# Kernel optimization log

Measured on AMD Instinct MI355X. Metric: run time of the kernel, lower is better.

## Reference

```python
import jax, jax.numpy as jnp
import numpy as np

N, E, DIN, H, DOUT = 100000, 400000, 128, 128, 128
LN_EPS = 1e-5


def _layernorm(x, g, b):
    m = jnp.mean(x, axis=-1, keepdims=True)
    v = jnp.mean((x - m) ** 2, axis=-1, keepdims=True)
    return (x - m) * jax.lax.rsqrt(v + LN_EPS) * g + b


def setup_inputs() -> dict:
    key = jax.random.key(0)
    ks = jax.random.split(key, 24)
    s = 1.0 / np.sqrt(H)
    inp = {
        'feat': jax.random.normal(ks[0], (N, DIN), jnp.float32),
        'edge_src': jax.random.randint(ks[1], (E,), 0, N, jnp.int32),
        'edge_dst': jax.random.randint(ks[2], (E,), 0, N, jnp.int32),
        'W_src': jax.random.normal(ks[3], (DIN, H), jnp.float32) * s,
        'b_src': jax.random.normal(ks[4], (H,), jnp.float32) * s,
        'W_dst': jax.random.normal(ks[5], (DIN, H), jnp.float32) * s,
        'b_dst': jax.random.normal(ks[6], (H,), jnp.float32) * s,
        'W1a': jax.random.normal(ks[7], (H, H), jnp.float32) * s,
        'W1b': jax.random.normal(ks[8], (H, H), jnp.float32) * s,
        'b1': jax.random.normal(ks[9], (H,), jnp.float32) * s,
        'W2': jax.random.normal(ks[10], (H, H), jnp.float32) * s,
        'b2': jax.random.normal(ks[11], (H,), jnp.float32) * s,
        'W3': jax.random.normal(ks[12], (H, H), jnp.float32) * s,
        'b3': jax.random.normal(ks[13], (H,), jnp.float32) * s,
        'ln_g': jnp.ones((H,), jnp.float32),
        'ln_b': jnp.zeros((H,), jnp.float32),
        'Wg1a': jax.random.normal(ks[14], (H, H), jnp.float32) * s,
        'Wg1b': jax.random.normal(ks[15], (H, H), jnp.float32) * s,
        'bg1': jax.random.normal(ks[16], (H,), jnp.float32) * s,
        'Wg2': jax.random.normal(ks[17], (H, 1), jnp.float32) * s,
        'bg2': jax.random.normal(ks[18], (1,), jnp.float32) * s,
        'W_out': jax.random.normal(ks[19], (H, DOUT), jnp.float32) * s,
        'b_out': jax.random.normal(ks[20], (DOUT,), jnp.float32) * s,
    }
    return inp


def reference(feat, edge_src, edge_dst, W_src, b_src, W_dst, b_dst,
              W1a, W1b, b1, W2, b2, W3, b3, ln_g, ln_b,
              Wg1a, Wg1b, bg1, Wg2, bg2, W_out, b_out):
    gelu = lambda x: jax.nn.gelu(x, approximate=False)  # torch nn.GELU default (erf)
    # node-level src/dst transforms, then gather per edge
    src_h = feat @ W_src + b_src                 # [N,H]
    dst_h = feat @ W_dst + b_dst                 # [N,H]
    se = src_h[edge_src]                         # [E,H]
    de = dst_h[edge_dst]                         # [E,H]
    # edge MLP on concat([se,de]) expressed as split weights (same math)
    h = gelu(se @ W1a + de @ W1b + b1)           # [E,H]
    h = gelu(h @ W2 + b2)                        # [E,H]
    msg = _layernorm(h @ W3 + b3, ln_g, ln_b)    # [E,H]
    # message gating
    gate = jax.nn.sigmoid(gelu(se @ Wg1a + de @ Wg1b + bg1) @ Wg2 + bg2)  # [E,1]
    msg = gate * msg
    # scatter-sum to destination nodes, then out transform
    upd = jax.ops.segment_sum(msg, edge_dst, num_segments=N)  # [N,H]
    return upd @ W_out + b_out                   # [N,DOUT]
```

## Files before the change

### kernel.cpp

```cpp
#include <hip/hip_runtime.h>
#include <hip/hip_bf16.h>
#include <math.h>


typedef __bf16 bf16x8 __attribute__((ext_vector_type(8)));
typedef __bf16 bf16x2 __attribute__((ext_vector_type(2)));
typedef float floatx4 __attribute__((ext_vector_type(4)));

#define LN_EPS 1e-5f

__device__ __forceinline__ unsigned short f2bf(float x) {
  unsigned int u = __float_as_uint(x);
  u = u + 0x7fffu + ((u >> 16) & 1u);
  return (unsigned short)(u >> 16);
}

__device__ __forceinline__ unsigned int pkbf(float lo, float hi) {
  bf16x2 v;
  v.x = (__bf16)lo;
  v.y = (__bf16)hi;
  return __builtin_bit_cast(unsigned int, v);
}

__device__ __forceinline__ unsigned short f2bfh(float x) {
  __bf16 h = (__bf16)x;
  return __builtin_bit_cast(unsigned short, h);
}

__device__ __forceinline__ float bf2f(unsigned short s) {
  return __uint_as_float(((unsigned int)s) << 16);
}

__device__ __forceinline__ float geluf(float x) {
  float t = x * x;
  float u = x * (2.3022080f + 0.1029434f * t);
  float e = __builtin_amdgcn_exp2f(-u);
  return x * __builtin_amdgcn_rcpf(1.0f + e);
}

__device__ __forceinline__ float sigmoidf_fast(float x) {
  float e = __builtin_amdgcn_exp2f(-1.44269504f * x);
  return __builtin_amdgcn_rcpf(1.0f + e);
}

__global__ __launch_bounds__(256) void prep_weights(
    const float* w0, const float* w1, const float* w2, const float* w3,
    const float* w4, const float* w5, const float* w6, const float* w7,
    const float* w8, unsigned short* out) {
  const float* srcs[9] = {w0, w1, w2, w3, w4, w5, w6, w7, w8};
  int m = blockIdx.x >> 2, c = blockIdx.x & 3;
  const float* src = srcs[m] + c * 32 * 128;
  __shared__ unsigned short sT[128][35];
  int tid = threadIdx.x;

  for (int it = 0; it < 4; ++it) {
    int f4 = tid + it * 256;
    float4 v = ((const float4*)src)[f4];
    int krel = f4 >> 5;
    int n0 = (f4 & 31) * 4;
    sT[n0 + 0][krel] = f2bf(v.x);
    sT[n0 + 1][krel] = f2bf(v.y);
    sT[n0 + 2][krel] = f2bf(v.z);
    sT[n0 + 3][krel] = f2bf(v.w);
  }
  __syncthreads();
  unsigned short* dst = out + m * 16384 + c * 32;
  for (int it = 0; it < 2; ++it) {
    int ch = tid + it * 256;
    int n = ch >> 2, kc = (ch & 3) * 8;
    unsigned short tmp[8];
    for (int j = 0; j < 8; ++j) tmp[j] = sT[n][kc + j];
    *(int4*)(dst + n * 128 + kc) = *(const int4*)tmp;
  }
}

#define LDB(pB, B)                                              \
  do {                                                          \
    const unsigned short* _p = (pB);                            \
    for (int kb = 0; kb < 4; ++kb) {                            \
      B[0][kb] = *(const bf16x8*)(_p + kb * 32);                \
      B[1][kb] = *(const bf16x8*)(_p + 2048 + kb * 32);         \
    }                                                           \
  } while (0)

__global__ __launch_bounds__(512, 8) void node_fused(
    const float* __restrict__ feat, const unsigned short* __restrict__ wT,
    const float* __restrict__ b_src, const float* __restrict__ b_dst,
    const float* __restrict__ b1, const float* __restrict__ bg1,
    unsigned short* __restrict__ SrcCat, unsigned short* __restrict__ DstCat,
    unsigned short* __restrict__ upd, int M) {
  __shared__ __align__(16) unsigned short sF[64][136];
  __shared__ __align__(16) unsigned short sT[64][136];
  int tid = threadIdx.x;
  int r0 = blockIdx.x * 64;
  int y = blockIdx.y;

  if (y == 0) {
    int4 z = {0, 0, 0, 0};
    int4* p = (int4*)(upd + (long long)r0 * 128);
    for (int it = 0; it < 2; ++it) {
      int idx = tid + it * 512;
      if (r0 + (idx >> 4) < M) p[idx] = z;
    }
  }

  {
    int r = tid >> 3, seg = tid & 7;
    int row = r0 + r;
    const float* src = feat + (long long)row * 128 + seg * 16;
    if (row < M) {
      float4 f0 = *(const float4*)(src);
      float4 f1 = *(const float4*)(src + 4);
      float4 f2 = *(const float4*)(src + 8);
      float4 f3 = *(const float4*)(src + 12);
      unsigned int t0[4] = {pkbf(f0.x, f0.y), pkbf(f0.z, f0.w),
                            pkbf(f1.x, f1.y), pkbf(f1.z, f1.w)};
      unsigned int t1[4] = {pkbf(f2.x, f2.y), pkbf(f2.z, f2.w),
                            pkbf(f3.x, f3.y), pkbf(f3.z, f3.w)};
      *(int4*)&sF[r][seg * 16] = *(const int4*)t0;
      *(int4*)&sF[r][seg * 16 + 8] = *(const int4*)t1;
    } else {
      int4 z = {0, 0, 0, 0};
      *(int4*)&sF[r][seg * 16] = z;
      *(int4*)&sF[r][seg * 16 + 8] = z;
    }
  }
  __syncthreads();

  int w = tid >> 6;
  int lane = tid & 63, lr = lane & 15, q = lane >> 4;
  int c0 = 16 * w + lr;
  const unsigned short* pB = wT + c0 * 128 + q * 8;

  const unsigned short* wH = pB + (y ? 1 : 0) * 16384;
  const unsigned short* wA = pB + (y ? 3 : 2) * 16384;
  const unsigned short* wG = pB + (y ? 7 : 6) * 16384;
  unsigned short* Cat = y ? DstCat : SrcCat;
  float hb = y ? b_dst[c0] : b_src[c0];
  float ab = y ? 0.f : b1[c0];
  float gb = y ? 0.f : bg1[c0];

  bf16x8 B[4];
  floatx4 acc[4];

  auto ldb = [&](const unsigned short* p) {
#pragma unroll
    for (int kb = 0; kb < 4; ++kb) B[kb] = *(const bf16x8*)(p + kb * 32);
  };
  auto zacc = [&]() {
#pragma unroll
    for (int mb = 0; mb < 4; ++mb) acc[mb] = (floatx4){0.f, 0.f, 0.f, 0.f};
  };
  auto pass = [&](const unsigned short (*Ab)[136]) {
#pragma unroll
    for (int kb = 0; kb < 4; ++kb) {
      int k = kb * 32 + q * 8;
#pragma unroll
      for (int mb = 0; mb < 4; ++mb) {
        bf16x8 a = *(const bf16x8*)&Ab[16 * mb + lr][k];
        acc[mb] = __builtin_amdgcn_mfma_f32_16x16x32_bf16(a, B[kb], acc[mb], 0, 0, 0);
      }
    }
  };
  auto stage = [&](unsigned short (*S)[136], float bv) {
#pragma unroll
    for (int mb = 0; mb < 4; ++mb)
#pragma unroll
      for (int i = 0; i < 4; ++i)
        S[16 * mb + 4 * q + i][c0] = f2bfh(acc[mb][i] + bv);
  };

  ldb(wH); zacc(); pass(sF); stage(sT, hb);
  __syncthreads();

  ldb(wA); zacc(); pass(sT); stage(sF, ab);
  ldb(wG); zacc(); pass(sT);
  __syncthreads();
  stage(sT, gb);
  __syncthreads();

  for (int it = 0; it < 4; ++it) {
    int idx = tid + it * 512;
    int row = idx >> 5, c = idx & 31;
    if (r0 + row < M) {
      const void* src = (c < 16) ? (const void*)&sF[row][c * 8]
                                 : (const void*)&sT[row][(c - 16) * 8];
      *(int4*)(Cat + (long long)(r0 + row) * 256 + c * 8) = *(const int4*)src;
    }
  }
}

__global__ __launch_bounds__(512, 8) void gemm_out(
    const unsigned short* __restrict__ A, const unsigned short* __restrict__ Bt,
    const float* __restrict__ bias, float* __restrict__ C, int M) {
  __shared__ __align__(16) char smem[64 * 130 * 4];
  unsigned short (*sA)[136] = (unsigned short(*)[136])smem;
  float (*sO)[130] = (float(*)[130])smem;
  int tid = threadIdx.x;
  int r0 = blockIdx.x * 64;

  for (int it = 0; it < 2; ++it) {
    int idx = tid + it * 512;
    int row = idx >> 4, c = idx & 15;
    int4 v = {0, 0, 0, 0};
    if (r0 + row < M) v = ((const int4*)(A + (long long)(r0 + row) * 128))[c];
    *(int4*)&sA[row][c * 8] = v;
  }
  __syncthreads();

  int w = tid >> 6, lane = tid & 63, lr = lane & 15, q = lane >> 4;
  int c0 = 16 * w + lr;
  const unsigned short* pB = Bt + c0 * 128 + q * 8;

  bf16x8 B[4];
#pragma unroll
  for (int kb = 0; kb < 4; ++kb) B[kb] = *(const bf16x8*)(pB + kb * 32);
  floatx4 acc[4];
#pragma unroll
  for (int mb = 0; mb < 4; ++mb) acc[mb] = (floatx4){0.f, 0.f, 0.f, 0.f};
#pragma unroll
  for (int kb = 0; kb < 4; ++kb) {
    int k = kb * 32 + q * 8;
#pragma unroll
    for (int mb = 0; mb < 4; ++mb) {
      bf16x8 a = *(const bf16x8*)&sA[16 * mb + lr][k];
      acc[mb] = __builtin_amdgcn_mfma_f32_16x16x32_bf16(a, B[kb], acc[mb], 0, 0, 0);
    }
  }
  __syncthreads();

  float bv = bias[c0];
#pragma unroll
  for (int mb = 0; mb < 4; ++mb)
#pragma unroll
    for (int i = 0; i < 4; ++i)
      sO[16 * mb + 4 * q + i][c0] = acc[mb][i] + bv;
  __syncthreads();

  for (int it = 0; it < 4; ++it) {
    int idx = tid + it * 512;
    int row = idx >> 5, c = idx & 31;
    if (r0 + row < M)
      *(float4*)(C + (long long)(r0 + row) * 128 + c * 4) = *(const float4*)&sO[row][c * 4];
  }
}

__global__ __launch_bounds__(256, 6) void edge_fused(
    const unsigned short* __restrict__ SrcCat, const unsigned short* __restrict__ DstCat,
    const int* __restrict__ edge_src, const int* __restrict__ edge_dst,
    const unsigned short* __restrict__ wT,
    const float* __restrict__ b2, const float* __restrict__ b3,
    const float* __restrict__ ln_g, const float* __restrict__ ln_b,
    const float* __restrict__ Wg2, const float* __restrict__ bg2,
    unsigned short* __restrict__ upd, int E) {
  __shared__ __align__(16) unsigned short sH[64][136];
  __shared__ int sDst[64];
  __shared__ float sGate[64];
  __shared__ float sR1[4][64];
  __shared__ float sR2[4][64];
  __shared__ float sM[64];
  __shared__ float sRS[64];

  int tid = threadIdx.x;
  int e0 = blockIdx.x * 64;

  {
    int r = tid >> 2, seg = tid & 3;
    int e = e0 + r;
    int ee = (e < E) ? e : (E - 1);
    int es = edge_src[ee], ed = edge_dst[ee];
    if (seg == 0) sDst[r] = (e < E) ? ed : -1;
    const unsigned short* ps = SrcCat + (long long)es * 256 + seg * 32;
    const unsigned short* pd = DstCat + (long long)ed * 256 + seg * 32;

    int4 sa[4], sb[4], ga[4], gb[4];
    for (int u = 0; u < 4; ++u) {
      sa[u] = ((const int4*)ps)[u];
      sb[u] = ((const int4*)pd)[u];
      ga[u] = ((const int4*)(ps + 128))[u];
      gb[u] = ((const int4*)(pd + 128))[u];
    }
    for (int u = 0; u < 4; ++u) {
      const unsigned short* av = (const unsigned short*)&sa[u];
      const unsigned short* bv = (const unsigned short*)&sb[u];
      unsigned int ov[4];
      for (int j = 0; j < 4; ++j) {
        float g0 = geluf(bf2f(av[2 * j])     + bf2f(bv[2 * j]));
        float g1 = geluf(bf2f(av[2 * j + 1]) + bf2f(bv[2 * j + 1]));
        ov[j] = pkbf(g0, g1);
      }
      *(int4*)&sH[r][seg * 32 + u * 8] = *(const int4*)ov;
    }
    float gp = 0.f;
    for (int u = 0; u < 4; ++u) {
      const unsigned short* av = (const unsigned short*)&ga[u];
      const unsigned short* bv = (const unsigned short*)&gb[u];
      float4 w0 = *(const float4*)(Wg2 + seg * 32 + u * 8);
      float4 w1 = *(const float4*)(Wg2 + seg * 32 + u * 8 + 4);
      gp += geluf(bf2f(av[0]) + bf2f(bv[0])) * w0.x;
      gp += geluf(bf2f(av[1]) + bf2f(bv[1])) * w0.y;
      gp += geluf(bf2f(av[2]) + bf2f(bv[2])) * w0.z;
      gp += geluf(bf2f(av[3]) + bf2f(bv[3])) * w0.w;
      gp += geluf(bf2f(av[4]) + bf2f(bv[4])) * w1.x;
      gp += geluf(bf2f(av[5]) + bf2f(bv[5])) * w1.y;
      gp += geluf(bf2f(av[6]) + bf2f(bv[6])) * w1.z;
      gp += geluf(bf2f(av[7]) + bf2f(bv[7])) * w1.w;
    }
    gp += __shfl_xor(gp, 1);
    gp += __shfl_xor(gp, 2);
    if (seg == 0) sGate[r] = sigmoidf_fast(gp + bg2[0]);
  }
  __syncthreads();

  int w = tid >> 6, lane = tid & 63, lr = lane & 15, q = lane >> 4;
  int c0 = 32 * w + lr, c1 = 32 * w + 16 + lr;
  const unsigned short* pB = wT + c0 * 128 + q * 8;

  bf16x8 B[2][4];
  floatx4 acc[4][2];
  auto zacc = [&]() {
    for (int mb = 0; mb < 4; ++mb)
      for (int nb = 0; nb < 2; ++nb) acc[mb][nb] = (floatx4){0.f, 0.f, 0.f, 0.f};
  };
  auto pass = [&](const unsigned short (*Ab)[136]) {
    for (int kb = 0; kb < 4; ++kb) {
      int k = kb * 32 + q * 8;
      for (int mb = 0; mb < 4; ++mb) {
        bf16x8 a = *(const bf16x8*)&Ab[16 * mb + lr][k];
        acc[mb][0] = __builtin_amdgcn_mfma_f32_16x16x32_bf16(a, B[0][kb], acc[mb][0], 0, 0, 0);
        acc[mb][1] = __builtin_amdgcn_mfma_f32_16x16x32_bf16(a, B[1][kb], acc[mb][1], 0, 0, 0);
      }
    }
  };

  LDB(pB + 4 * 16384, B);
  zacc();
  pass(sH);
  __syncthreads();
  {
    float bv0 = b2[c0], bv1 = b2[c1];
    for (int mb = 0; mb < 4; ++mb)
      for (int i = 0; i < 4; ++i) {
        int r = 16 * mb + 4 * q + i;
        unsigned int u = pkbf(geluf(acc[mb][0][i] + bv0), geluf(acc[mb][1][i] + bv1));
        sH[r][c0] = (unsigned short)u;
        sH[r][c1] = (unsigned short)(u >> 16);
      }
  }
  __syncthreads();

  LDB(pB + 5 * 16384, B);
  zacc();
  pass(sH);
  {
    float bv0 = b3[c0], bv1 = b3[c1];
    for (int mb = 0; mb < 4; ++mb)
      for (int i = 0; i < 4; ++i) {
        float x0 = acc[mb][0][i] + bv0;
        float x1 = acc[mb][1][i] + bv1;
        acc[mb][0][i] = x0; acc[mb][1][i] = x1;
        float s = x0 + x1, s2 = x0 * x0 + x1 * x1;
        s += __shfl_xor(s, 1); s += __shfl_xor(s, 2);
        s += __shfl_xor(s, 4); s += __shfl_xor(s, 8);
        s2 += __shfl_xor(s2, 1); s2 += __shfl_xor(s2, 2);
        s2 += __shfl_xor(s2, 4); s2 += __shfl_xor(s2, 8);
        if (lr == 0) { sR1[w][16 * mb + 4 * q + i] = s; sR2[w][16 * mb + 4 * q + i] = s2; }
      }
  }
  __syncthreads();
  if (tid < 64) {
    float s = sR1[0][tid] + sR1[1][tid] + sR1[2][tid] + sR1[3][tid];
    float s2 = sR2[0][tid] + sR2[1][tid] + sR2[2][tid] + sR2[3][tid];
    float m = s * (1.f / 128.f);
    float v = s2 * (1.f / 128.f) - m * m;
    sM[tid] = m;
    sRS[tid] = rsqrtf(v + LN_EPS);
  }
  __syncthreads();

  {
    float lg0 = ln_g[c0], lg1 = ln_g[c1];
    float lb0 = ln_b[c0], lb1 = ln_b[c1];
    for (int mb = 0; mb < 4; ++mb)
      for (int i = 0; i < 4; ++i) {
        int r = 16 * mb + 4 * q + i;
        int dst = sDst[r];
        float m = sM[r], rs = sRS[r], gt = sGate[r];
        float v0 = ((acc[mb][0][i] - m) * rs * lg0 + lb0) * gt;
        float v1 = ((acc[mb][1][i] - m) * rs * lg1 + lb1) * gt;
        float o0 = __shfl_xor(v0, 1);
        float o1 = __shfl_xor(v1, 1);
        if (dst >= 0) {
          unsigned int pk;
          int colb;
          if ((lr & 1) == 0) {
            pk = pkbf(v0, o0);
            colb = c0;
          } else {
            pk = pkbf(o1, v1);
            colb = c0 + 15;
          }
          unsigned short* addr = upd + (long long)dst * 128 + colb;
          asm volatile("global_atomic_pk_add_bf16 %0, %1, off"
                       :: "v"(addr), "v"(pk) : "memory");
        }
      }
  }
}

extern "C" void kernel_launch(void* const* d_in, const int* in_sizes, int n_in,
                              void* d_out, int out_size, void* d_ws, size_t ws_size,
                              hipStream_t stream) {
  const float* feat   = (const float*)d_in[0];
  const int* edge_src = (const int*)d_in[1];
  const int* edge_dst = (const int*)d_in[2];
  const float* W_src = (const float*)d_in[3];  const float* b_src = (const float*)d_in[4];
  const float* W_dst = (const float*)d_in[5];  const float* b_dst = (const float*)d_in[6];
  const float* W1a = (const float*)d_in[7];    const float* W1b = (const float*)d_in[8];
  const float* b1  = (const float*)d_in[9];
  const float* W2  = (const float*)d_in[10];   const float* b2  = (const float*)d_in[11];
  const float* W3  = (const float*)d_in[12];   const float* b3  = (const float*)d_in[13];
  const float* ln_g = (const float*)d_in[14];  const float* ln_b = (const float*)d_in[15];
  const float* Wg1a = (const float*)d_in[16];  const float* Wg1b = (const float*)d_in[17];
  const float* bg1  = (const float*)d_in[18];
  const float* Wg2  = (const float*)d_in[19];  const float* bg2 = (const float*)d_in[20];
  const float* W_out = (const float*)d_in[21]; const float* b_out = (const float*)d_in[22];

  int N = in_sizes[0] / 128;
  int E = in_sizes[1];

  char* ws = (char*)d_ws;
  unsigned short* wT = (unsigned short*)ws;
  size_t off = 9 * 16384 * sizeof(unsigned short);
  unsigned short* SrcCat = (unsigned short*)(ws + off);
  off += (size_t)N * 256 * sizeof(unsigned short);
  unsigned short* DstCat = (unsigned short*)(ws + off);
  off += (size_t)N * 256 * sizeof(unsigned short);
  unsigned short* upd = (unsigned short*)(ws + off);

  prep_weights<<<36, 256, 0, stream>>>(W_src, W_dst, W1a, W1b, W2, W3, Wg1a, Wg1b,
                                       W_out, wT);
  int mtiles = (N + 63) / 64;
  node_fused<<<dim3(mtiles, 2), 512, 0, stream>>>(feat, wT, b_src, b_dst, b1, bg1,
                                                  SrcCat, DstCat, upd, N);
  edge_fused<<<(E + 63) / 64, 256, 0, stream>>>(SrcCat, DstCat, edge_src, edge_dst,
                                                wT, b2, b3, ln_g, ln_b, Wg2, bg2,
                                                upd, E);
  gemm_out<<<mtiles, 512, 0, stream>>>(upd, wT + 8 * 16384, b_out, (float*)d_out, N);
}
```

Baseline: 350.9 us.

## Bucket-sort edges by destination block and remap edge tiles per XCD

Adds a counting sort (histogram, single-block scan, atomic scatter) that groups edges by destination node in buckets of 64. The edge kernel then reads edges through this permutation, so scatter-add atomics into upd land on nearby rows and DstCat gathers gain locality. The edge kernel's block-to-tile mapping is also remapped so consecutive tiles go to the same XCD, aiming to keep L2 reuse for destination rows. The cost is three extra small kernels, a memset and one more indirection per edge. The scan is limited to 2048 buckets, which covers N=100000 (1563 buckets) but no larger N.

```diff
diff --git a/kernel.cpp b/kernel.cpp
--- a/kernel.cpp
+++ b/kernel.cpp
@@ -82,6 +82,42 @@
       B[1][kb] = *(const bf16x8*)(_p + 2048 + kb * 32);         \
     }                                                           \
   } while (0)
+
+__global__ __launch_bounds__(256) void ehist(
+    const int* __restrict__ edge_dst, int* __restrict__ hist, int E) {
+  int i = blockIdx.x * 256 + threadIdx.x;
+  if (i < E) atomicAdd(&hist[edge_dst[i] >> 6], 1);
+}
+
+__global__ __launch_bounds__(256) void escan(
+    const int* __restrict__ hist, int* __restrict__ offs, int nb) {
+  __shared__ int tmp[2048];
+  int tid = threadIdx.x;
+  for (int i = tid; i < 2048; i += 256) tmp[i] = (i < nb) ? hist[i] : 0;
+  __syncthreads();
+  for (int d = 1; d < 2048; d <<= 1) {
+    int vals[8];
+    for (int j = 0; j < 8; ++j) {
+      int i = tid + j * 256;
+      vals[j] = (i >= d) ? tmp[i - d] : 0;
+    }
+    __syncthreads();
+    for (int j = 0; j < 8; ++j) tmp[tid + j * 256] += vals[j];
+    __syncthreads();
+  }
+  for (int i = tid; i < 2048; i += 256)
+    offs[i] = tmp[i] - ((i < nb) ? hist[i] : 0);
+}
+
+__global__ __launch_bounds__(256) void escatter(
+    const int* __restrict__ edge_dst, int* __restrict__ offs,
+    int* __restrict__ perm, int E) {
+  int i = blockIdx.x * 256 + threadIdx.x;
+  if (i < E) {
+    int pos = atomicAdd(&offs[edge_dst[i] >> 6], 1);
+    perm[pos] = i;
+  }
+}
 
 __global__ __launch_bounds__(512, 8) void node_fused(
     const float* __restrict__ feat, const unsigned short* __restrict__ wT,
@@ -248,6 +284,7 @@
 __global__ __launch_bounds__(256, 6) void edge_fused(
     const unsigned short* __restrict__ SrcCat, const unsigned short* __restrict__ DstCat,
     const int* __restrict__ edge_src, const int* __restrict__ edge_dst,
+    const int* __restrict__ perm,
     const unsigned short* __restrict__ wT,
     const float* __restrict__ b2, const float* __restrict__ b3,
     const float* __restrict__ ln_g, const float* __restrict__ ln_b,
@@ -262,12 +299,17 @@
   __shared__ float sRS[64];
 
   int tid = threadIdx.x;
-  int e0 = blockIdx.x * 64;
+  int nwg = gridDim.x;
+  int bq = nwg >> 3, br = nwg & 7;
+  int xcd = blockIdx.x & 7, j = blockIdx.x >> 3;
+  int wk = (xcd < br) ? xcd * (bq + 1) + j : br * (bq + 1) + (xcd - br) * bq + j;
+  int e0 = wk * 64;
 
   {
     int r = tid >> 2, seg = tid & 3;
     int e = e0 + r;
     int ee = (e < E) ? e : (E - 1);
+    if (perm) ee = perm[ee];
     int es = edge_src[ee], ed = edge_dst[ee];
     if (seg == 0) sDst[r] = (e < E) ? ed : -1;
     const unsigned short* ps = SrcCat + (long long)es * 256 + seg * 32;
@@ -284,10 +326,10 @@
       const unsigned short* av = (const unsigned short*)&sa[u];
       const unsigned short* bv = (const unsigned short*)&sb[u];
       unsigned int ov[4];
-      for (int j = 0; j < 4; ++j) {
-        float g0 = geluf(bf2f(av[2 * j])     + bf2f(bv[2 * j]));
-        float g1 = geluf(bf2f(av[2 * j + 1]) + bf2f(bv[2 * j + 1]));
-        ov[j] = pkbf(g0, g1);
+      for (int j2 = 0; j2 < 4; ++j2) {
+        float g0 = geluf(bf2f(av[2 * j2])     + bf2f(bv[2 * j2]));
+        float g1 = geluf(bf2f(av[2 * j2 + 1]) + bf2f(bv[2 * j2 + 1]));
+        ov[j2] = pkbf(g0, g1);
       }
       *(int4*)&sH[r][seg * 32 + u * 8] = *(const int4*)ov;
     }
@@ -437,13 +479,28 @@
   unsigned short* DstCat = (unsigned short*)(ws + off);
   off += (size_t)N * 256 * sizeof(unsigned short);
   unsigned short* upd = (unsigned short*)(ws + off);
+  off += (size_t)N * 128 * sizeof(unsigned short);
+  int* perm = (int*)(ws + off);
+  size_t off_perm_end = off + (size_t)E * sizeof(int);
+  int* hist = (int*)(ws + off_perm_end);
+  int* offs = hist + 2048;
+  size_t need = off_perm_end + 2 * 2048 * sizeof(int);
+  bool use_sort = (ws_size >= need);
 
   prep_weights<<<36, 256, 0, stream>>>(W_src, W_dst, W1a, W1b, W2, W3, Wg1a, Wg1b,
                                        W_out, wT);
   int mtiles = (N + 63) / 64;
   node_fused<<<dim3(mtiles, 2), 512, 0, stream>>>(feat, wT, b_src, b_dst, b1, bg1,
                                                   SrcCat, DstCat, upd, N);
+  if (use_sort) {
+    int nb = (N + 63) / 64;
+    hipMemsetAsync(hist, 0, 2048 * sizeof(int), stream);
+    ehist<<<(E + 255) / 256, 256, 0, stream>>>(edge_dst, hist, E);
+    escan<<<1, 256, 0, stream>>>(hist, offs, nb);
+    escatter<<<(E + 255) / 256, 256, 0, stream>>>(edge_dst, offs, perm, E);
+  }
   edge_fused<<<(E + 63) / 64, 256, 0, stream>>>(SrcCat, DstCat, edge_src, edge_dst,
+                                                use_sort ? perm : nullptr,
                                                 wT, b2, b3, ln_g, ln_b, Wg2, bg2,
                                                 upd, E);
   gemm_out<<<mtiles, 512, 0, stream>>>(upd, wT + 8 * 16384, b_out, (float*)d_out, N);
```

Result: slower. 479.6 us (+36.7%).
